# Kernel optimization log

Measured on AMD Instinct MI355X. Metric: run time of the kernel, lower is better.

## Reference

```python
import jax, jax.numpy as jnp
import numpy as np

HEADS = 8


def setup_inputs() -> dict:
    key = jax.random.key(0)
    ks = jax.random.split(key, 5)
    B, C, H, W = 2, 256, 48, 48
    s = 0.02
    return {
        "ct": jax.random.normal(ks[0], (B, C, H, W), jnp.float32),
        "us": jax.random.normal(ks[1], (B, C, H, W), jnp.float32),
        "w_qkv_ct": jax.random.normal(ks[2], (3 * C, C), jnp.float32) * s,
        "w_qkv_us": jax.random.normal(ks[3], (3 * C, C), jnp.float32) * s,
        "w_proj": jax.random.normal(ks[4], (C, 2 * C), jnp.float32) * s,
        "b_proj": jnp.zeros((C,), jnp.float32),
    }


def _heads_view(x, B, H, W):
    # [B, C, H, W] -> [B, heads, HW, dh]
    C = x.shape[1]
    return x.reshape(B, HEADS, C // HEADS, H * W).transpose(0, 1, 3, 2)


def _cross_attn(q, k, v, scale):
    # q,k,v: [B, heads, HW, dh]
    attn = jax.nn.softmax(jnp.einsum("bhnd,bhmd->bhnm", q, k) * scale, axis=-1)
    return jnp.einsum("bhnm,bhmd->bhnd", attn, v)


def reference(ct, us, w_qkv_ct, w_qkv_us, w_proj, b_proj):
    B, C, H, W = ct.shape
    dh = C // HEADS
    scale = dh ** (-0.5)

    # 1x1 convs as channel GEMMs
    qkv1 = jnp.einsum("oc,bchw->bohw", w_qkv_ct, ct)
    qkv2 = jnp.einsum("oc,bchw->bohw", w_qkv_us, us)
    q1, k1, v1 = jnp.split(qkv1, 3, axis=1)
    q2, k2, v2 = jnp.split(qkv2, 3, axis=1)

    # CT queries attend to US keys/values
    o1 = _cross_attn(_heads_view(q1, B, H, W), _heads_view(k2, B, H, W),
                     _heads_view(v2, B, H, W), scale)
    # US queries attend to CT keys/values
    o2 = _cross_attn(_heads_view(q2, B, H, W), _heads_view(k1, B, H, W),
                     _heads_view(v1, B, H, W), scale)

    # [B, heads, HW, dh] -> [B, C, H, W]
    out1 = o1.transpose(0, 1, 3, 2).reshape(B, C, H, W)
    out2 = o2.transpose(0, 1, 3, 2).reshape(B, C, H, W)

    fused = jnp.concatenate([ct + out1, us + out2], axis=1)
    return jnp.einsum("oc,bchw->bohw", w_proj, fused) + b_proj[None, :, None, None]
```

## Files before the change

### kernel.cpp

```cpp
#include <hip/hip_runtime.h>
#include <hip/hip_bf16.h>
#include <math.h>

#define HW   2304
#define CCH  256

#define QSCALE 0.25504368686637270f

typedef short short8 __attribute__((ext_vector_type(8)));
typedef float f32x4  __attribute__((ext_vector_type(4)));

__device__ inline unsigned short f2bf(float f) {
    union { float f; unsigned u; } v; v.f = f;
    unsigned r = v.u + 0x7FFF + ((v.u >> 16) & 1);
    return (unsigned short)(r >> 16);
}
__device__ inline unsigned pkbf2(float a, float b) {
    float2 f; f.x = a; f.y = b;
    union { __hip_bfloat162 h; unsigned u; } c;
    c.h = __float22bfloat162_rn(f);
    return c.u;
}
__device__ inline unsigned pktrunc(float a, float b) {
    return __builtin_amdgcn_perm(__builtin_bit_cast(unsigned, b),
                                 __builtin_bit_cast(unsigned, a), 0x07060302u);
}

__global__ __launch_bounds__(256, 4) void prep_k(
    const float* __restrict__ ct, const float* __restrict__ us,
    const float* __restrict__ w1, const float* __restrict__ w2,
    const float* __restrict__ w3,
    unsigned short* __restrict__ xT,
    unsigned short* __restrict__ b1, unsigned short* __restrict__ b2,
    unsigned short* __restrict__ b3)
{
    const int bx = blockIdx.x, t = threadIdx.x;
    if (bx >= 576) {
        const int u = bx - 576;
        int z, base;
        if (u < 192)      { z = 0; base = u * 1024; }
        else if (u < 384) { z = 1; base = (u - 192) * 1024; }
        else              { z = 2; base = (u - 384) * 1024; }
        const float* s = (z == 0) ? w1 : (z == 1) ? w2 : w3;
        unsigned short* d = (z == 0) ? b1 : (z == 1) ? b2 : b3;
        const int i = base + t * 4;
        const float4 v = *(const float4*)&s[i];
        const float sc = (z < 2 && i < 65536) ? QSCALE : 1.f;
        uint2 p; p.x = pkbf2(v.x * sc, v.y * sc); p.y = pkbf2(v.z * sc, v.w * sc);
        *(uint2*)&d[i] = p;
        return;
    }
    const int pt = bx % 36, rest = bx / 36, ctile = rest & 3, z = rest >> 2;
    const float* __restrict__ src = ((z >> 1) ? us : ct) + (size_t)(z & 1) * CCH * HW;
    unsigned short* __restrict__ dst = xT + (size_t)z * HW * 256;
    const int p0 = pt * 64, c0 = ctile * 64;
    __shared__ __align__(16) unsigned short Ts[64 * 72];
#pragma unroll
    for (int r = 0; r < 4; r++) {
        const int c = (t >> 4) + 16 * r;
        const float4 v = *(const float4*)&src[(size_t)(c0 + c) * HW + p0 + (t & 15) * 4];
        Ts[((t & 15) * 4 + 0) * 72 + c] = f2bf(v.x);
        Ts[((t & 15) * 4 + 1) * 72 + c] = f2bf(v.y);
        Ts[((t & 15) * 4 + 2) * 72 + c] = f2bf(v.z);
        Ts[((t & 15) * 4 + 3) * 72 + c] = f2bf(v.w);
    }
    __syncthreads();
    const int p = t >> 2, c8 = (t & 3) * 16;
    const short8 a  = *(const short8*)&Ts[p * 72 + c8];
    const short8 b8 = *(const short8*)&Ts[p * 72 + c8 + 8];
    *(short8*)&dst[(size_t)(p0 + p) * 256 + c0 + c8]     = a;
    *(short8*)&dst[(size_t)(p0 + p) * 256 + c0 + c8 + 8] = b8;
}

__global__ __launch_bounds__(256, 4) void qkv_k(
    const unsigned short* __restrict__ xT,
    const unsigned short* __restrict__ wb1, const unsigned short* __restrict__ wb2,
    unsigned short* __restrict__ qkvT1, unsigned short* __restrict__ qkvT2,
    unsigned short* __restrict__ vdm1,  unsigned short* __restrict__ vdm2)
{
    const int inp = blockIdx.z >> 1, b = blockIdx.z & 1;
    const unsigned short* __restrict__ X = xT + (size_t)(inp * 2 + b) * HW * 256;
    const unsigned short* __restrict__ W = inp ? wb2 : wb1;
    unsigned short* __restrict__ qT = (inp ? qkvT2 : qkvT1) + (size_t)b * HW * 512;
    unsigned short* __restrict__ vd = (inp ? vdm2 : vdm1) + (size_t)b * CCH * HW;
    const int p0 = blockIdx.x * 64, o0 = blockIdx.y * 64;

    __shared__ __align__(16) unsigned short Ws[64 * 72];
    __shared__ __align__(16) unsigned short Xs[64 * 72];
    const int t = threadIdx.x, w = t >> 6, lane = t & 63, quad = lane >> 4, m = lane & 15;
    const int sr = t >> 3, sc = t & 7;

    f32x4 acc[4] = {{0,0,0,0},{0,0,0,0},{0,0,0,0},{0,0,0,0}};

    for (int k0 = 0; k0 < 256; k0 += 64) {
        const short8 wv0 = *(const short8*)&W[(size_t)(o0 + sr) * 256 + k0 + sc * 8];
        const short8 wv1 = *(const short8*)&W[(size_t)(o0 + 32 + sr) * 256 + k0 + sc * 8];
        const short8 xv0 = *(const short8*)&X[(size_t)(p0 + sr) * 256 + k0 + sc * 8];
        const short8 xv1 = *(const short8*)&X[(size_t)(p0 + 32 + sr) * 256 + k0 + sc * 8];
        __syncthreads();
        *(short8*)&Ws[sr * 72 + sc * 8] = wv0;
        *(short8*)&Ws[(32 + sr) * 72 + sc * 8] = wv1;
        *(short8*)&Xs[sr * 72 + sc * 8] = xv0;
        *(short8*)&Xs[(32 + sr) * 72 + sc * 8] = xv1;
        __syncthreads();
#pragma unroll
        for (int kc2 = 0; kc2 < 2; kc2++) {
            const short8 af = *(const short8*)&Ws[(w * 16 + m) * 72 + kc2 * 32 + quad * 8];
#pragma unroll
            for (int pg = 0; pg < 4; pg++) {
                const short8 bf = *(const short8*)&Xs[(pg * 16 + m) * 72 + kc2 * 32 + quad * 8];
                acc[pg] = __builtin_amdgcn_mfma_f32_16x16x32_bf16(af, bf, acc[pg], 0, 0, 0);
            }
        }
    }

    __syncthreads();
    if (o0 < 512) {
#pragma unroll
        for (int pg = 0; pg < 4; pg++) {
            uint2 pk; pk.x = pkbf2(acc[pg][0], acc[pg][1]); pk.y = pkbf2(acc[pg][2], acc[pg][3]);
            *(uint2*)&Ws[(pg * 16 + m) * 72 + w * 16 + quad * 4] = pk;
        }
        __syncthreads();
        const int pr = t >> 2, cc = t & 3;
        const uint4 d0 = *(const uint4*)&Ws[pr * 72 + cc * 16];
        const uint4 d1 = *(const uint4*)&Ws[pr * 72 + cc * 16 + 8];
        *(uint4*)&qT[(size_t)(p0 + pr) * 512 + o0 + cc * 16]     = d0;
        *(uint4*)&qT[(size_t)(p0 + pr) * 512 + o0 + cc * 16 + 8] = d1;
    } else {
#pragma unroll
        for (int pg = 0; pg < 4; pg++)
#pragma unroll
            for (int r = 0; r < 4; r++)
                Ws[(w * 16 + quad * 4 + r) * 72 + pg * 16 + m] = f2bf(acc[pg][r]);
        __syncthreads();
        const int dr = t >> 2, cc = t & 3;
        const uint4 d0 = *(const uint4*)&Ws[dr * 72 + cc * 16];
        const uint4 d1 = *(const uint4*)&Ws[dr * 72 + cc * 16 + 8];
        *(uint4*)&vd[(size_t)(o0 - 512 + dr) * HW + p0 + cc * 16]     = d0;
        *(uint4*)&vd[(size_t)(o0 - 512 + dr) * HW + p0 + cc * 16 + 8] = d1;
    }
}

#define KS_STR 80
#define VS_STR 136
__global__ __launch_bounds__(256, 5) void attn_k(
    const unsigned short* __restrict__ qkvT1, const unsigned short* __restrict__ qkvT2,
    const unsigned short* __restrict__ vdm1,  const unsigned short* __restrict__ vdm2,
    const float* __restrict__ ct, const float* __restrict__ us,
    unsigned short* __restrict__ fusedT)
{
    const int dir = blockIdx.z, b = blockIdx.y >> 3, h = blockIdx.y & 7;
    const unsigned short* __restrict__ Qt = (dir ? qkvT2 : qkvT1) + (size_t)b * HW * 512;
    const unsigned short* __restrict__ Kt = (dir ? qkvT1 : qkvT2) + (size_t)b * HW * 512
                                            + 256 + h * 32;
    const unsigned short* __restrict__ Vd = (dir ? vdm1 : vdm2) + ((size_t)b * CCH + h * 32) * HW;
    const float* __restrict__ src = (dir ? us : ct) + ((size_t)b * CCH + h * 32) * HW;

    const int t = threadIdx.x, w = t >> 6, lane = t & 63, quad = lane >> 4, m = lane & 15;

    __shared__ __align__(16) unsigned short Ks[128 * KS_STR];
    __shared__ __align__(16) unsigned short Vs[32 * VS_STR];

    const int pq = blockIdx.x * 64 + w * 16 + m;
    const short8 qf = *(const short8*)&Qt[(size_t)pq * 512 + h * 32 + quad * 8];

    f32x4 acc0 = {0,0,0,0}, acc1 = {0,0,0,0}, accl = {0,0,0,0};
    const short ONE = (short)0x3F80;
    const short8 ones = {ONE,ONE,ONE,ONE,ONE,ONE,ONE,ONE};

    const int kj0 = t >> 2, kcs = t & 3;
    const int vr0 = t >> 4, vcs = t & 15;
    const unsigned short* __restrict__ ksb = &Ks[((m >> 2) * 8 + (m & 3)) * KS_STR + quad * 8];
    const unsigned short* __restrict__ vsb = &Vs[m * VS_STR + quad * 8];

    for (int j0 = 0; j0 < HW; j0 += 128) {
        const short8 ka = *(const short8*)&Kt[(size_t)(j0 + kj0) * 512 + kcs * 8];
        const short8 kb = *(const short8*)&Kt[(size_t)(j0 + kj0 + 64) * 512 + kcs * 8];
        const short8 va = *(const short8*)&Vd[(size_t)vr0 * HW + j0 + vcs * 8];
        const short8 vb = *(const short8*)&Vd[(size_t)(vr0 + 16) * HW + j0 + vcs * 8];
        __syncthreads();
        *(short8*)&Ks[kj0 * KS_STR + kcs * 8] = ka;
        *(short8*)&Ks[(kj0 + 64) * KS_STR + kcs * 8] = kb;
        *(short8*)&Vs[vr0 * VS_STR + vcs * 8] = va;
        *(short8*)&Vs[(vr0 + 16) * VS_STR + vcs * 8] = vb;
        __syncthreads();

        uint4 pw4[4];
#pragma unroll
        for (int f = 0; f < 8; f++) {
            const short8 kf = *(const short8*)(ksb + ((f >> 1) * 32 + (f & 1) * 4) * KS_STR);
            const f32x4 z = {0,0,0,0};
            const f32x4 S = __builtin_amdgcn_mfma_f32_16x16x32_bf16(kf, qf, z, 0, 0, 0);
            const float e0 = __builtin_amdgcn_exp2f(S[0]);
            const float e1 = __builtin_amdgcn_exp2f(S[1]);
            const float e2 = __builtin_amdgcn_exp2f(S[2]);
            const float e3 = __builtin_amdgcn_exp2f(S[3]);
            if ((f & 1) == 0) { pw4[f >> 1].x = pktrunc(e0, e1); pw4[f >> 1].y = pktrunc(e2, e3); }
            else              { pw4[f >> 1].z = pktrunc(e0, e1); pw4[f >> 1].w = pktrunc(e2, e3); }
        }

#pragma unroll
        for (int kt = 0; kt < 4; kt++) {
            const short8 pf = __builtin_bit_cast(short8, pw4[kt]);
            const short8 vf0 = *(const short8*)(vsb + kt * 32);
            const short8 vf1 = *(const short8*)(vsb + 16 * VS_STR + kt * 32);
            acc0 = __builtin_amdgcn_mfma_f32_16x16x32_bf16(vf0, pf, acc0, 0, 0, 0);
            acc1 = __builtin_amdgcn_mfma_f32_16x16x32_bf16(vf1, pf, acc1, 0, 0, 0);
            accl = __builtin_amdgcn_mfma_f32_16x16x32_bf16(ones, pf, accl, 0, 0, 0);
        }
    }

    const float inv = 1.f / accl[0];

    const int cb = dir * 256 + h * 32, d0 = quad * 4;
    unsigned short* __restrict__ fT = fusedT + ((size_t)b * HW + pq) * 512 + cb + d0;
    uint2 s0, s1;
    s0.x = pkbf2(acc0[0] * inv + src[(size_t)(d0 + 0) * HW + pq],
                 acc0[1] * inv + src[(size_t)(d0 + 1) * HW + pq]);
    s0.y = pkbf2(acc0[2] * inv + src[(size_t)(d0 + 2) * HW + pq],
                 acc0[3] * inv + src[(size_t)(d0 + 3) * HW + pq]);
    s1.x = pkbf2(acc1[0] * inv + src[(size_t)(16 + d0 + 0) * HW + pq],
                 acc1[1] * inv + src[(size_t)(16 + d0 + 1) * HW + pq]);
    s1.y = pkbf2(acc1[2] * inv + src[(size_t)(16 + d0 + 2) * HW + pq],
                 acc1[3] * inv + src[(size_t)(16 + d0 + 3) * HW + pq]);
    *(uint2*)&fT[0]  = s0;
    *(uint2*)&fT[16] = s1;
}

__global__ __launch_bounds__(256, 4) void proj_k(
    const unsigned short* __restrict__ w3b, const unsigned short* __restrict__ fusedT,
    const float* __restrict__ bias, float* __restrict__ out)
{
    const int p0 = blockIdx.x * 64, o0 = blockIdx.y * 64;
    __shared__ __align__(16) unsigned short Ws[64 * 72];
    __shared__ __align__(16) unsigned short Xs[64 * 72];
    const int t = threadIdx.x, w = t >> 6, lane = t & 63, quad = lane >> 4, m = lane & 15;
    const int sr = t >> 3, sc = t & 7;

    f32x4 acc[4] = {{0,0,0,0},{0,0,0,0},{0,0,0,0},{0,0,0,0}};

    for (int k0 = 0; k0 < 512; k0 += 64) {
        const short8 wv0 = *(const short8*)&w3b[(size_t)(o0 + sr) * 512 + k0 + sc * 8];
        const short8 wv1 = *(const short8*)&w3b[(size_t)(o0 + 32 + sr) * 512 + k0 + sc * 8];
        const short8 xv0 = *(const short8*)&fusedT[(size_t)(p0 + sr) * 512 + k0 + sc * 8];
        const short8 xv1 = *(const short8*)&fusedT[(size_t)(p0 + 32 + sr) * 512 + k0 + sc * 8];
        __syncthreads();
        *(short8*)&Ws[sr * 72 + sc * 8] = wv0;
        *(short8*)&Ws[(32 + sr) * 72 + sc * 8] = wv1;
        *(short8*)&Xs[sr * 72 + sc * 8] = xv0;
        *(short8*)&Xs[(32 + sr) * 72 + sc * 8] = xv1;
        __syncthreads();
#pragma unroll
        for (int kc2 = 0; kc2 < 2; kc2++) {
            const short8 af = *(const short8*)&Ws[(w * 16 + m) * 72 + kc2 * 32 + quad * 8];
#pragma unroll
            for (int pg = 0; pg < 4; pg++) {
                const short8 bf = *(const short8*)&Xs[(pg * 16 + m) * 72 + kc2 * 32 + quad * 8];
                acc[pg] = __builtin_amdgcn_mfma_f32_16x16x32_bf16(af, bf, acc[pg], 0, 0, 0);
            }
        }
    }

    const int b = (p0 >= HW) ? 1 : 0;
    const int pl0 = p0 - b * HW;
    float* __restrict__ ob = out + (size_t)b * CCH * HW;
    float b4[4];
#pragma unroll
    for (int r = 0; r < 4; r++) b4[r] = bias[o0 + w * 16 + quad * 4 + r];
#pragma unroll
    for (int pg = 0; pg < 4; pg++)
#pragma unroll
        for (int r = 0; r < 4; r++)
            ob[(size_t)(o0 + w * 16 + quad * 4 + r) * HW + pl0 + pg * 16 + m]
                = acc[pg][r] + b4[r];
}

extern "C" void kernel_launch(void* const* d_in, const int* in_sizes, int n_in,
                              void* d_out, int out_size, void* d_ws, size_t ws_size,
                              hipStream_t stream)
{
    const float* ct       = (const float*)d_in[0];
    const float* us       = (const float*)d_in[1];
    const float* w_qkv_ct = (const float*)d_in[2];
    const float* w_qkv_us = (const float*)d_in[3];
    const float* w_proj   = (const float*)d_in[4];
    const float* b_proj   = (const float*)d_in[5];
    float* out = (float*)d_out;

    unsigned short* wb1   = (unsigned short*)d_ws;
    unsigned short* wb2   = wb1 + (size_t)768 * 256;
    unsigned short* w3b   = wb2 + (size_t)768 * 256;
    unsigned short* xT    = w3b + (size_t)256 * 512;
    unsigned short* qkvT1 = xT    + (size_t)4 * HW * 256;
    unsigned short* qkvT2 = qkvT1 + (size_t)2 * HW * 512;
    unsigned short* vdm1  = qkvT2 + (size_t)2 * HW * 512;
    unsigned short* vdm2  = vdm1  + (size_t)2 * CCH * HW;
    unsigned short* fusedT= vdm2  + (size_t)2 * CCH * HW;

    prep_k<<<dim3(1088), 256, 0, stream>>>(ct, us, w_qkv_ct, w_qkv_us, w_proj,
                                           xT, wb1, wb2, w3b);
    qkv_k <<<dim3(36, 12, 4), 256, 0, stream>>>(xT, wb1, wb2, qkvT1, qkvT2, vdm1, vdm2);
    attn_k<<<dim3(36, 16, 2), 256, 0, stream>>>(qkvT1, qkvT2, vdm1, vdm2, ct, us, fusedT);
    proj_k<<<dim3(72, 4), 256, 0, stream>>>(w3b, fusedT, b_proj, out);
}
```

Baseline: 126.1 us.

## Fuse bf16 conversion of inputs and weights into GEMMs and swizzle K tile

Removes the separate prep kernel that transposed ct/us to bf16 and converted the weights. The QKV and projection GEMMs now read fp32 activations and weights directly, converting and transposing into shared memory in the load stage, and the Q scale is applied on the fly. The attention kernel's K shared tile drops its padded stride in favour of an XOR swizzle to avoid bank conflicts. In exchange, each GEMM block re-reads fp32 data (twice the bytes) and repeats the weight conversion, and the transposing LDS stores use narrower writes.

Result: slower. 140.0 us (+11.0%).

```diff
diff --git a/kernel.cpp b/kernel.cpp
--- a/kernel.cpp
+++ b/kernel.cpp
@@ -26,61 +26,15 @@
                                  __builtin_bit_cast(unsigned, a), 0x07060302u);
 }
 
-__global__ __launch_bounds__(256, 4) void prep_k(
+__global__ __launch_bounds__(256, 4) void qkv_k(
     const float* __restrict__ ct, const float* __restrict__ us,
-    const float* __restrict__ w1, const float* __restrict__ w2,
-    const float* __restrict__ w3,
-    unsigned short* __restrict__ xT,
-    unsigned short* __restrict__ b1, unsigned short* __restrict__ b2,
-    unsigned short* __restrict__ b3)
-{
-    const int bx = blockIdx.x, t = threadIdx.x;
-    if (bx >= 576) {
-        const int u = bx - 576;
-        int z, base;
-        if (u < 192)      { z = 0; base = u * 1024; }
-        else if (u < 384) { z = 1; base = (u - 192) * 1024; }
-        else              { z = 2; base = (u - 384) * 1024; }
-        const float* s = (z == 0) ? w1 : (z == 1) ? w2 : w3;
-        unsigned short* d = (z == 0) ? b1 : (z == 1) ? b2 : b3;
-        const int i = base + t * 4;
-        const float4 v = *(const float4*)&s[i];
-        const float sc = (z < 2 && i < 65536) ? QSCALE : 1.f;
-        uint2 p; p.x = pkbf2(v.x * sc, v.y * sc); p.y = pkbf2(v.z * sc, v.w * sc);
-        *(uint2*)&d[i] = p;
-        return;
-    }
-    const int pt = bx % 36, rest = bx / 36, ctile = rest & 3, z = rest >> 2;
-    const float* __restrict__ src = ((z >> 1) ? us : ct) + (size_t)(z & 1) * CCH * HW;
-    unsigned short* __restrict__ dst = xT + (size_t)z * HW * 256;
-    const int p0 = pt * 64, c0 = ctile * 64;
-    __shared__ __align__(16) unsigned short Ts[64 * 72];
-#pragma unroll
-    for (int r = 0; r < 4; r++) {
-        const int c = (t >> 4) + 16 * r;
-        const float4 v = *(const float4*)&src[(size_t)(c0 + c) * HW + p0 + (t & 15) * 4];
-        Ts[((t & 15) * 4 + 0) * 72 + c] = f2bf(v.x);
-        Ts[((t & 15) * 4 + 1) * 72 + c] = f2bf(v.y);
-        Ts[((t & 15) * 4 + 2) * 72 + c] = f2bf(v.z);
-        Ts[((t & 15) * 4 + 3) * 72 + c] = f2bf(v.w);
-    }
-    __syncthreads();
-    const int p = t >> 2, c8 = (t & 3) * 16;
-    const short8 a  = *(const short8*)&Ts[p * 72 + c8];
-    const short8 b8 = *(const short8*)&Ts[p * 72 + c8 + 8];
-    *(short8*)&dst[(size_t)(p0 + p) * 256 + c0 + c8]     = a;
-    *(short8*)&dst[(size_t)(p0 + p) * 256 + c0 + c8 + 8] = b8;
-}
-
-__global__ __launch_bounds__(256, 4) void qkv_k(
-    const unsigned short* __restrict__ xT,
-    const unsigned short* __restrict__ wb1, const unsigned short* __restrict__ wb2,
+    const float* __restrict__ w_ct, const float* __restrict__ w_us,
     unsigned short* __restrict__ qkvT1, unsigned short* __restrict__ qkvT2,
     unsigned short* __restrict__ vdm1,  unsigned short* __restrict__ vdm2)
 {
     const int inp = blockIdx.z >> 1, b = blockIdx.z & 1;
-    const unsigned short* __restrict__ X = xT + (size_t)(inp * 2 + b) * HW * 256;
-    const unsigned short* __restrict__ W = inp ? wb2 : wb1;
+    const float* __restrict__ X = (inp ? us : ct) + (size_t)b * CCH * HW;
+    const float* __restrict__ W = inp ? w_us : w_ct;
     unsigned short* __restrict__ qT = (inp ? qkvT2 : qkvT1) + (size_t)b * HW * 512;
     unsigned short* __restrict__ vd = (inp ? vdm2 : vdm1) + (size_t)b * CCH * HW;
     const int p0 = blockIdx.x * 64, o0 = blockIdx.y * 64;
@@ -88,20 +42,37 @@
     __shared__ __align__(16) unsigned short Ws[64 * 72];
     __shared__ __align__(16) unsigned short Xs[64 * 72];
     const int t = threadIdx.x, w = t >> 6, lane = t & 63, quad = lane >> 4, m = lane & 15;
-    const int sr = t >> 3, sc = t & 7;
+
+    const int wo = t >> 2, wc = (t & 3) * 16;
+    const int pg8 = t & 15, cg = t >> 4;
+    const float sc = (o0 < 256) ? QSCALE : 1.0f;
 
     f32x4 acc[4] = {{0,0,0,0},{0,0,0,0},{0,0,0,0},{0,0,0,0}};
 
     for (int k0 = 0; k0 < 256; k0 += 64) {
-        const short8 wv0 = *(const short8*)&W[(size_t)(o0 + sr) * 256 + k0 + sc * 8];
-        const short8 wv1 = *(const short8*)&W[(size_t)(o0 + 32 + sr) * 256 + k0 + sc * 8];
-        const short8 xv0 = *(const short8*)&X[(size_t)(p0 + sr) * 256 + k0 + sc * 8];
-        const short8 xv1 = *(const short8*)&X[(size_t)(p0 + 32 + sr) * 256 + k0 + sc * 8];
-        __syncthreads();
-        *(short8*)&Ws[sr * 72 + sc * 8] = wv0;
-        *(short8*)&Ws[(32 + sr) * 72 + sc * 8] = wv1;
-        *(short8*)&Xs[sr * 72 + sc * 8] = xv0;
-        *(short8*)&Xs[(32 + sr) * 72 + sc * 8] = xv1;
+        float4 wv[4];
+#pragma unroll
+        for (int i = 0; i < 4; i++)
+            wv[i] = *(const float4*)&W[(size_t)(o0 + wo) * 256 + k0 + wc + 4 * i];
+        float4 xv[4];
+#pragma unroll
+        for (int i = 0; i < 4; i++)
+            xv[i] = *(const float4*)&X[(size_t)(k0 + cg * 4 + i) * HW + p0 + pg8 * 4];
+        __syncthreads();
+        uint4 wp0, wp1;
+        wp0.x = pkbf2(wv[0].x * sc, wv[0].y * sc); wp0.y = pkbf2(wv[0].z * sc, wv[0].w * sc);
+        wp0.z = pkbf2(wv[1].x * sc, wv[1].y * sc); wp0.w = pkbf2(wv[1].z * sc, wv[1].w * sc);
+        wp1.x = pkbf2(wv[2].x * sc, wv[2].y * sc); wp1.y = pkbf2(wv[2].z * sc, wv[2].w * sc);
+        wp1.z = pkbf2(wv[3].x * sc, wv[3].y * sc); wp1.w = pkbf2(wv[3].z * sc, wv[3].w * sc);
+        *(uint4*)&Ws[wo * 72 + wc]     = wp0;
+        *(uint4*)&Ws[wo * 72 + wc + 8] = wp1;
+#pragma unroll
+        for (int j = 0; j < 4; j++) {
+            uint2 q;
+            q.x = pkbf2(((const float*)&xv[0])[j], ((const float*)&xv[1])[j]);
+            q.y = pkbf2(((const float*)&xv[2])[j], ((const float*)&xv[3])[j]);
+            *(uint2*)&Xs[(pg8 * 4 + j) * 72 + cg * 4] = q;
+        }
         __syncthreads();
 #pragma unroll
         for (int kc2 = 0; kc2 < 2; kc2++) {
@@ -142,7 +113,7 @@
     }
 }
 
-#define KS_STR 80
+#define KS_STR 64
 #define VS_STR 136
 __global__ __launch_bounds__(256, 5) void attn_k(
     const unsigned short* __restrict__ qkvT1, const unsigned short* __restrict__ qkvT2,
@@ -170,8 +141,10 @@
     const short8 ones = {ONE,ONE,ONE,ONE,ONE,ONE,ONE,ONE};
 
     const int kj0 = t >> 2, kcs = t & 3;
+    const int pcK = kcs ^ ((kj0 >> 3) & 3);
     const int vr0 = t >> 4, vcs = t & 15;
-    const unsigned short* __restrict__ ksb = &Ks[((m >> 2) * 8 + (m & 3)) * KS_STR + quad * 8];
+    const unsigned short* __restrict__ ksb =
+        &Ks[(((m >> 2) * 8 + (m & 3)) * KS_STR) + ((quad ^ (m >> 2)) * 8)];
     const unsigned short* __restrict__ vsb = &Vs[m * VS_STR + quad * 8];
 
     for (int j0 = 0; j0 < HW; j0 += 128) {
@@ -180,8 +153,8 @@
         const short8 va = *(const short8*)&Vd[(size_t)vr0 * HW + j0 + vcs * 8];
         const short8 vb = *(const short8*)&Vd[(size_t)(vr0 + 16) * HW + j0 + vcs * 8];
         __syncthreads();
-        *(short8*)&Ks[kj0 * KS_STR + kcs * 8] = ka;
-        *(short8*)&Ks[(kj0 + 64) * KS_STR + kcs * 8] = kb;
+        *(short8*)&Ks[kj0 * KS_STR + pcK * 8] = ka;
+        *(short8*)&Ks[(kj0 + 64) * KS_STR + pcK * 8] = kb;
         *(short8*)&Vs[vr0 * VS_STR + vcs * 8] = va;
         *(short8*)&Vs[(vr0 + 16) * VS_STR + vcs * 8] = vb;
         __syncthreads();
@@ -229,25 +202,33 @@
 }
 
 __global__ __launch_bounds__(256, 4) void proj_k(
-    const unsigned short* __restrict__ w3b, const unsigned short* __restrict__ fusedT,
+    const float* __restrict__ w3, const unsigned short* __restrict__ fusedT,
     const float* __restrict__ bias, float* __restrict__ out)
 {
     const int p0 = blockIdx.x * 64, o0 = blockIdx.y * 64;
     __shared__ __align__(16) unsigned short Ws[64 * 72];
     __shared__ __align__(16) unsigned short Xs[64 * 72];
     const int t = threadIdx.x, w = t >> 6, lane = t & 63, quad = lane >> 4, m = lane & 15;
+    const int wo = t >> 2, wc = (t & 3) * 16;
     const int sr = t >> 3, sc = t & 7;
 
     f32x4 acc[4] = {{0,0,0,0},{0,0,0,0},{0,0,0,0},{0,0,0,0}};
 
     for (int k0 = 0; k0 < 512; k0 += 64) {
-        const short8 wv0 = *(const short8*)&w3b[(size_t)(o0 + sr) * 512 + k0 + sc * 8];
-        const short8 wv1 = *(const short8*)&w3b[(size_t)(o0 + 32 + sr) * 512 + k0 + sc * 8];
+        float4 wv[4];
+#pragma unroll
+        for (int i = 0; i < 4; i++)
+            wv[i] = *(const float4*)&w3[(size_t)(o0 + wo) * 512 + k0 + wc + 4 * i];
         const short8 xv0 = *(const short8*)&fusedT[(size_t)(p0 + sr) * 512 + k0 + sc * 8];
         const short8 xv1 = *(const short8*)&fusedT[(size_t)(p0 + 32 + sr) * 512 + k0 + sc * 8];
         __syncthreads();
-        *(short8*)&Ws[sr * 72 + sc * 8] = wv0;
-        *(short8*)&Ws[(32 + sr) * 72 + sc * 8] = wv1;
+        uint4 wp0, wp1;
+        wp0.x = pkbf2(wv[0].x, wv[0].y); wp0.y = pkbf2(wv[0].z, wv[0].w);
+        wp0.z = pkbf2(wv[1].x, wv[1].y); wp0.w = pkbf2(wv[1].z, wv[1].w);
+        wp1.x = pkbf2(wv[2].x, wv[2].y); wp1.y = pkbf2(wv[2].z, wv[2].w);
+        wp1.z = pkbf2(wv[3].x, wv[3].y); wp1.w = pkbf2(wv[3].z, wv[3].w);
+        *(uint4*)&Ws[wo * 72 + wc]     = wp0;
+        *(uint4*)&Ws[wo * 72 + wc + 8] = wp1;
         *(short8*)&Xs[sr * 72 + sc * 8] = xv0;
         *(short8*)&Xs[(32 + sr) * 72 + sc * 8] = xv1;
         __syncthreads();
@@ -288,19 +269,14 @@
     const float* b_proj   = (const float*)d_in[5];
     float* out = (float*)d_out;
 
-    unsigned short* wb1   = (unsigned short*)d_ws;
-    unsigned short* wb2   = wb1 + (size_t)768 * 256;
-    unsigned short* w3b   = wb2 + (size_t)768 * 256;
-    unsigned short* xT    = w3b + (size_t)256 * 512;
-    unsigned short* qkvT1 = xT    + (size_t)4 * HW * 256;
+    unsigned short* qkvT1 = (unsigned short*)d_ws;
     unsigned short* qkvT2 = qkvT1 + (size_t)2 * HW * 512;
     unsigned short* vdm1  = qkvT2 + (size_t)2 * HW * 512;
     unsigned short* vdm2  = vdm1  + (size_t)2 * CCH * HW;
     unsigned short* fusedT= vdm2  + (size_t)2 * CCH * HW;
 
-    prep_k<<<dim3(1088), 256, 0, stream>>>(ct, us, w_qkv_ct, w_qkv_us, w_proj,
-                                           xT, wb1, wb2, w3b);
-    qkv_k <<<dim3(36, 12, 4), 256, 0, stream>>>(xT, wb1, wb2, qkvT1, qkvT2, vdm1, vdm2);
+    qkv_k <<<dim3(36, 12, 4), 256, 0, stream>>>(ct, us, w_qkv_ct, w_qkv_us,
+                                                qkvT1, qkvT2, vdm1, vdm2);
     attn_k<<<dim3(36, 16, 2), 256, 0, stream>>>(qkvT1, qkvT2, vdm1, vdm2, ct, us, fusedT);
-    proj_k<<<dim3(72, 4), 256, 0, stream>>>(w3b, fusedT, b_proj, out);
-}
+    proj_k<<<dim3(72, 4), 256, 0, stream>>>(w_proj, fusedT, b_proj, out);
+}
```

## Load V fragments directly from global and XOR-swizzle unpadded K tile in LDS

Applied to the files above, without the earlier changes.

The attention kernel no longer stages V through shared memory. Each lane loads its V MFMA fragments straight from global memory into registers. The K tile drops its padded stride in favour of a dense 32-element row with an XOR swizzle to avoid bank conflicts. This shrinks LDS use per block and removes the V LDS writes and reads. In exchange, each wave redundantly fetches V from global/L2 and holds more registers, which may hurt occupancy under the 5-block launch bound.

Measured after the change: 177.6 us. 1.41x slower.

```diff
diff --git a/kernel.cpp b/kernel.cpp
--- a/kernel.cpp
+++ b/kernel.cpp
@@ -142,8 +142,6 @@
     }
 }
 
-#define KS_STR 80
-#define VS_STR 136
 __global__ __launch_bounds__(256, 5) void attn_k(
     const unsigned short* __restrict__ qkvT1, const unsigned short* __restrict__ qkvT2,
     const unsigned short* __restrict__ vdm1,  const unsigned short* __restrict__ vdm2,
@@ -159,8 +157,7 @@
 
     const int t = threadIdx.x, w = t >> 6, lane = t & 63, quad = lane >> 4, m = lane & 15;
 
-    __shared__ __align__(16) unsigned short Ks[128 * KS_STR];
-    __shared__ __align__(16) unsigned short Vs[32 * VS_STR];
+    __shared__ __align__(16) unsigned short Ks[128 * 32];
 
     const int pq = blockIdx.x * 64 + w * 16 + m;
     const short8 qf = *(const short8*)&Qt[(size_t)pq * 512 + h * 32 + quad * 8];
@@ -170,26 +167,31 @@
     const short8 ones = {ONE,ONE,ONE,ONE,ONE,ONE,ONE,ONE};
 
     const int kj0 = t >> 2, kcs = t & 3;
-    const int vr0 = t >> 4, vcs = t & 15;
-    const unsigned short* __restrict__ ksb = &Ks[((m >> 2) * 8 + (m & 3)) * KS_STR + quad * 8];
-    const unsigned short* __restrict__ vsb = &Vs[m * VS_STR + quad * 8];
+    const int pcK = kcs ^ (((kj0 >> 1) & 1) | (((kj0 >> 3) & 1) << 1));
+    const int g2m = ((m >> 1) & 1) | (((m >> 2) & 1) << 1);
+    const unsigned short* __restrict__ ksb =
+        &Ks[((m >> 2) * 8 + (m & 3)) * 32 + (quad ^ g2m) * 8];
+    const unsigned short* __restrict__ vp0 = Vd + (size_t)m * HW + quad * 8;
+    const unsigned short* __restrict__ vp1 = Vd + (size_t)(16 + m) * HW + quad * 8;
 
     for (int j0 = 0; j0 < HW; j0 += 128) {
         const short8 ka = *(const short8*)&Kt[(size_t)(j0 + kj0) * 512 + kcs * 8];
         const short8 kb = *(const short8*)&Kt[(size_t)(j0 + kj0 + 64) * 512 + kcs * 8];
-        const short8 va = *(const short8*)&Vd[(size_t)vr0 * HW + j0 + vcs * 8];
-        const short8 vb = *(const short8*)&Vd[(size_t)(vr0 + 16) * HW + j0 + vcs * 8];
-        __syncthreads();
-        *(short8*)&Ks[kj0 * KS_STR + kcs * 8] = ka;
-        *(short8*)&Ks[(kj0 + 64) * KS_STR + kcs * 8] = kb;
-        *(short8*)&Vs[vr0 * VS_STR + vcs * 8] = va;
-        *(short8*)&Vs[(vr0 + 16) * VS_STR + vcs * 8] = vb;
+        short8 vg0[4], vg1[4];
+#pragma unroll
+        for (int kt = 0; kt < 4; kt++) {
+            vg0[kt] = *(const short8*)(vp0 + j0 + kt * 32);
+            vg1[kt] = *(const short8*)(vp1 + j0 + kt * 32);
+        }
+        __syncthreads();
+        *(short8*)&Ks[kj0 * 32 + pcK * 8] = ka;
+        *(short8*)&Ks[(kj0 + 64) * 32 + pcK * 8] = kb;
         __syncthreads();
 
         uint4 pw4[4];
 #pragma unroll
         for (int f = 0; f < 8; f++) {
-            const short8 kf = *(const short8*)(ksb + ((f >> 1) * 32 + (f & 1) * 4) * KS_STR);
+            const short8 kf = *(const short8*)(ksb + ((f >> 1) * 32 + (f & 1) * 4) * 32);
             const f32x4 z = {0,0,0,0};
             const f32x4 S = __builtin_amdgcn_mfma_f32_16x16x32_bf16(kf, qf, z, 0, 0, 0);
             const float e0 = __builtin_amdgcn_exp2f(S[0]);
@@ -203,10 +205,8 @@
 #pragma unroll
         for (int kt = 0; kt < 4; kt++) {
             const short8 pf = __builtin_bit_cast(short8, pw4[kt]);
-            const short8 vf0 = *(const short8*)(vsb + kt * 32);
-            const short8 vf1 = *(const short8*)(vsb + 16 * VS_STR + kt * 32);
-            acc0 = __builtin_amdgcn_mfma_f32_16x16x32_bf16(vf0, pf, acc0, 0, 0, 0);
-            acc1 = __builtin_amdgcn_mfma_f32_16x16x32_bf16(vf1, pf, acc1, 0, 0, 0);
+            acc0 = __builtin_amdgcn_mfma_f32_16x16x32_bf16(vg0[kt], pf, acc0, 0, 0, 0);
+            acc1 = __builtin_amdgcn_mfma_f32_16x16x32_bf16(vg1[kt], pf, acc1, 0, 0, 0);
             accl = __builtin_amdgcn_mfma_f32_16x16x32_bf16(ones, pf, accl, 0, 0, 0);
         }
     }
```
